# Kernel tuning notes

Measured on AMD Instinct MI355X. Metric: run time of the kernel, lower is better.

The kernel has to match this reference:

```python
import jax, jax.numpy as jnp
import numpy as np

K = 32  # neighbors per point (self.k)

def setup_inputs() -> dict:
    key = jax.random.key(0)
    k1, k2 = jax.random.split(key)
    B, N, C = 16, 4096, 64
    x = jax.random.normal(k1, (B, N, C), dtype=jnp.float32)
    idx = jax.random.randint(k2, (B, N, K), 0, N, dtype=jnp.int64)
    return {"x": x, "idx": idx}

def reference(x, idx):
    # pooled[b, n, :] = mean_k x[b, idx[b, n, k], :]
    # gather per-batch: xb[ib] -> [N, K, C]
    gathered = jax.vmap(lambda xb, ib: xb[ib])(x, idx)  # [B, N, K, C]
    return gathered.mean(axis=2)  # [B, N, C]
```

## Files before the change

### kernel.cpp

```cpp
#include <hip/hip_runtime.h>


#define BB 16
#define NN 4096
#define KK 32
#define CC 64
#define CH8 8
#define NCHUNK (CC / CH8)
#define NQ 4
#define PTS (NN / NQ)
#define THREADS 512
#define IDX16_ELEMS (BB * NN * KK)

__device__ __forceinline__ uint pk_bf16(float a, float b) {
    uint ua = __float_as_uint(a);
    ua = (ua + 0x7fffu + ((ua >> 16) & 1u)) >> 16;
    uint ub = __float_as_uint(b);
    ub = (ub + 0x7fffu + ((ub >> 16) & 1u)) & 0xffff0000u;
    return ua | ub;
}

__global__ __launch_bounds__(256)
void prep_kernel(const float* __restrict__ x,
                 const int* __restrict__ idx32,
                 ushort* __restrict__ idx16,
                 uint4* __restrict__ xbf) {
    int vprobe = idx32[2 * (threadIdx.x & 63) + 1];
    const int is64 = (__ballot(vprobe != 0) == 0ULL) ? 1 : 0;

    const int tid = blockIdx.x * blockDim.x + threadIdx.x;
    const int stride = gridDim.x * blockDim.x;

    if (is64) {
        const int4* __restrict__ in = (const int4*)idx32;
        uint* __restrict__ o = (uint*)idx16;
        for (int i = tid; i < IDX16_ELEMS / 2; i += stride) {
            int4 v = in[i];
            o[i] = (uint)(v.x & 0xFFFF) | ((uint)(v.z & 0xFFFF) << 16);
        }
    } else {
        const int4* __restrict__ in = (const int4*)idx32;
        uint2* __restrict__ o = (uint2*)idx16;
        for (int i = tid; i < IDX16_ELEMS / 4; i += stride) {
            int4 v = in[i];
            o[i] = make_uint2((uint)(v.x & 0xFFFF) | ((uint)(v.y & 0xFFFF) << 16),
                              (uint)(v.z & 0xFFFF) | ((uint)(v.w & 0xFFFF) << 16));
        }
    }

    const float4* __restrict__ x4 = (const float4*)x;
    for (int row = tid; row < BB * NN; row += stride) {
        const size_t base = (size_t)row * (CC / 4);
        const int b = row >> 12;
        const int n = row & (NN - 1);
#pragma unroll
        for (int ch = 0; ch < NCHUNK; ++ch) {
            const float4 v0 = x4[base + ch * 2];
            const float4 v1 = x4[base + ch * 2 + 1];
            xbf[(size_t)(b * NCHUNK + ch) * NN + n] =
                make_uint4(pk_bf16(v0.x, v0.y), pk_bf16(v0.z, v0.w),
                           pk_bf16(v1.x, v1.y), pk_bf16(v1.z, v1.w));
        }
    }
}

__device__ __forceinline__ void acc8(float a[8], uint4 r) {
    a[0] += __uint_as_float(r.x << 16);
    a[1] += __uint_as_float(r.x & 0xffff0000u);
    a[2] += __uint_as_float(r.y << 16);
    a[3] += __uint_as_float(r.y & 0xffff0000u);
    a[4] += __uint_as_float(r.z << 16);
    a[5] += __uint_as_float(r.z & 0xffff0000u);
    a[6] += __uint_as_float(r.w << 16);
    a[7] += __uint_as_float(r.w & 0xffff0000u);
}

__global__ __launch_bounds__(THREADS, 4)
void gapool_bf16_kernel(const ushort* __restrict__ idx16,
                        const uint4* __restrict__ xbf,
                        float* __restrict__ out) {
    __shared__ uint4 tile[NN];

    const int bid = blockIdx.x;
    const int b = bid & 15;
    const int g = bid >> 4;
    const int chunk = g & (NCHUNK - 1);
    const int q = g >> 3;
    const int tid = threadIdx.x;
    const float s = 1.0f / KK;

    const ushort* __restrict__ idxq =
        idx16 + ((size_t)b * NN + (size_t)q * PTS) * KK;
    float* __restrict__ outq =
        out + ((size_t)b * NN + (size_t)q * PTS) * CC + chunk * CH8;
    const uint4* __restrict__ src = xbf + (size_t)(b * NCHUNK + chunk) * NN;

    const uint4* __restrict__ ip0 = (const uint4*)(idxq + (size_t)tid * KK);
    uint4 pa = ip0[0], pb = ip0[1], pc = ip0[2], pd = ip0[3];

    for (int r = tid; r < NN; r += THREADS) tile[r] = src[r];
    __syncthreads();

    for (int p = tid; p < PTS; p += THREADS) {
        const uint w[16] = {pa.x, pa.y, pa.z, pa.w, pb.x, pb.y, pb.z, pb.w,
                            pc.x, pc.y, pc.z, pc.w, pd.x, pd.y, pd.z, pd.w};
        if (p + THREADS < PTS) {
            const uint4* ipn =
                (const uint4*)(idxq + (size_t)(p + THREADS) * KK);
            pa = ipn[0]; pb = ipn[1]; pc = ipn[2]; pd = ipn[3];
        }

        float a[8] = {0.f, 0.f, 0.f, 0.f, 0.f, 0.f, 0.f, 0.f};
#pragma unroll
        for (int i = 0; i < 16; ++i) {
            acc8(a, tile[w[i] & 0xFFFFu]);
            acc8(a, tile[w[i] >> 16]);
        }

        float4* op = (float4*)(outq + (size_t)p * CC);
        op[0] = make_float4(a[0] * s, a[1] * s, a[2] * s, a[3] * s);
        op[1] = make_float4(a[4] * s, a[5] * s, a[6] * s, a[7] * s);
    }
}

extern "C" void kernel_launch(void* const* d_in, const int* in_sizes, int n_in,
                              void* d_out, int out_size, void* d_ws, size_t ws_size,
                              hipStream_t stream) {
    const float* x     = (const float*)d_in[0];
    const int*   idx32 = (const int*)d_in[1];
    float*       out   = (float*)d_out;
    ushort*      idx16 = (ushort*)d_ws;
    uint4*       xbf   = (uint4*)((char*)d_ws + IDX16_ELEMS * 2);

    prep_kernel<<<256, 256, 0, stream>>>(x, idx32, idx16, xbf);

    gapool_bf16_kernel<<<BB * NCHUNK * NQ, THREADS, 0, stream>>>(
        idx16, xbf, out);
}
```

Baseline: 89.34 us.

## Fuse x bf16 conversion into pooling kernel and widen index-pack grid

Drops the separate pass that converts x to a chunk-major bf16 workspace. Each pooling block now reads its fp32 channel slice of x straight from global memory and packs it to bf16 while filling the shared tile. The index-packing kernel gets a much larger grid (2048 blocks instead of 256). This saves a global write and re-read of the bf16 copy. In exchange, each block does strided 32-byte reads from fp32 rows, and each x row is read by the four point-quarter blocks, which costs more read bandwidth in the gather kernel.

```diff
diff --git a/kernel.cpp b/kernel.cpp
--- a/kernel.cpp
+++ b/kernel.cpp
@@ -21,10 +21,8 @@
 }
 
 __global__ __launch_bounds__(256)
-void prep_kernel(const float* __restrict__ x,
-                 const int* __restrict__ idx32,
-                 ushort* __restrict__ idx16,
-                 uint4* __restrict__ xbf) {
+void pack_idx_kernel(const int* __restrict__ idx32,
+                     ushort* __restrict__ idx16) {
     int vprobe = idx32[2 * (threadIdx.x & 63) + 1];
     const int is64 = (__ballot(vprobe != 0) == 0ULL) ? 1 : 0;
 
@@ -47,21 +45,6 @@
                               (uint)(v.z & 0xFFFF) | ((uint)(v.w & 0xFFFF) << 16));
         }
     }
-
-    const float4* __restrict__ x4 = (const float4*)x;
-    for (int row = tid; row < BB * NN; row += stride) {
-        const size_t base = (size_t)row * (CC / 4);
-        const int b = row >> 12;
-        const int n = row & (NN - 1);
-#pragma unroll
-        for (int ch = 0; ch < NCHUNK; ++ch) {
-            const float4 v0 = x4[base + ch * 2];
-            const float4 v1 = x4[base + ch * 2 + 1];
-            xbf[(size_t)(b * NCHUNK + ch) * NN + n] =
-                make_uint4(pk_bf16(v0.x, v0.y), pk_bf16(v0.z, v0.w),
-                           pk_bf16(v1.x, v1.y), pk_bf16(v1.z, v1.w));
-        }
-    }
 }
 
 __device__ __forceinline__ void acc8(float a[8], uint4 r) {
@@ -76,9 +59,9 @@
 }
 
 __global__ __launch_bounds__(THREADS, 4)
-void gapool_bf16_kernel(const ushort* __restrict__ idx16,
-                        const uint4* __restrict__ xbf,
-                        float* __restrict__ out) {
+void gapool_fused_kernel(const float* __restrict__ x,
+                         const ushort* __restrict__ idx16,
+                         float* __restrict__ out) {
     __shared__ uint4 tile[NN];
 
     const int bid = blockIdx.x;
@@ -93,12 +76,18 @@
         idx16 + ((size_t)b * NN + (size_t)q * PTS) * KK;
     float* __restrict__ outq =
         out + ((size_t)b * NN + (size_t)q * PTS) * CC + chunk * CH8;
-    const uint4* __restrict__ src = xbf + (size_t)(b * NCHUNK + chunk) * NN;
 
     const uint4* __restrict__ ip0 = (const uint4*)(idxq + (size_t)tid * KK);
     uint4 pa = ip0[0], pb = ip0[1], pc = ip0[2], pd = ip0[3];
 
-    for (int r = tid; r < NN; r += THREADS) tile[r] = src[r];
+    const float4* __restrict__ xsrc =
+        (const float4*)(x + (size_t)b * NN * CC + chunk * CH8);
+    for (int r = tid; r < NN; r += THREADS) {
+        const float4 v0 = xsrc[(size_t)r * (CC / 4)];
+        const float4 v1 = xsrc[(size_t)r * (CC / 4) + 1];
+        tile[r] = make_uint4(pk_bf16(v0.x, v0.y), pk_bf16(v0.z, v0.w),
+                             pk_bf16(v1.x, v1.y), pk_bf16(v1.z, v1.w));
+    }
     __syncthreads();
 
     for (int p = tid; p < PTS; p += THREADS) {
@@ -130,10 +119,9 @@
     const int*   idx32 = (const int*)d_in[1];
     float*       out   = (float*)d_out;
     ushort*      idx16 = (ushort*)d_ws;
-    uint4*       xbf   = (uint4*)((char*)d_ws + IDX16_ELEMS * 2);
 
-    prep_kernel<<<256, 256, 0, stream>>>(x, idx32, idx16, xbf);
+    pack_idx_kernel<<<2048, 256, 0, stream>>>(idx32, idx16);
 
-    gapool_bf16_kernel<<<BB * NCHUNK * NQ, THREADS, 0, stream>>>(
-        idx16, xbf, out);
+    gapool_fused_kernel<<<BB * NCHUNK * NQ, THREADS, 0, stream>>>(
+        x, idx16, out);
 }
```

Result: no change. 91.06 us (+1.9%).
